# Optimization experiments

Measured on AMD Instinct MI355X. Metric: run time of the kernel, lower is better.

The kernel has to match this reference:

```python
import jax, jax.numpy as jnp
import numpy as np

N, E, IN, H, L, C, K, OPS, B, OUT = 50000, 800000, 64, 128, 3, 4, 32, 7, 512, 10
D = 2 * H * (L + 1)  # classifier in_dim


def _seg_sum(v, idx, n):
    return jax.ops.segment_sum(v, idx, num_segments=n)


def setup_inputs() -> dict:
    key = jax.random.key(0)
    ks = jax.random.split(key, 12)
    s = 0.05
    inp = {}
    inp["x"] = jax.random.normal(ks[0], (N, IN), jnp.float32)
    inp["edge_index"] = jax.random.randint(ks[1], (2, E), 0, N)
    inp["batch"] = jnp.sort(jax.random.randint(ks[2], (N,), 0, B))
    inp["lin1_W"] = jax.random.normal(ks[3], (IN, H), jnp.float32) * s
    inp["lin1_b"] = jnp.zeros((H,), jnp.float32)
    inp["vn0"] = jnp.zeros((H,), jnp.float32)  # virtualnode_embedding init zeros
    inp["W_ops"] = jax.random.normal(ks[4], (L, C, OPS, H, K), jnp.float32) * s
    inp["b_ops"] = jnp.zeros((L, C, OPS, K), jnp.float32)
    inp["att_a"] = jax.random.normal(ks[5], (L, 2, H), jnp.float32) * s
    inp["ln_g"] = jnp.ones((L, C, K), jnp.float32)
    inp["ln_b"] = jnp.zeros((L, C, K), jnp.float32)
    inp["bn_g"] = jnp.ones((L, H), jnp.float32)
    inp["bn_b"] = jnp.zeros((L, H), jnp.float32)
    inp["vn_W1"] = jax.random.normal(ks[6], (L - 1, H, 2 * H), jnp.float32) * s
    inp["vn_b1"] = jnp.zeros((L - 1, 2 * H), jnp.float32)
    inp["vn_bn1_g"] = jnp.ones((L - 1, 2 * H), jnp.float32)
    inp["vn_bn1_b"] = jnp.zeros((L - 1, 2 * H), jnp.float32)
    inp["vn_W2"] = jax.random.normal(ks[7], (L - 1, 2 * H, H), jnp.float32) * s
    inp["vn_b2"] = jnp.zeros((L - 1, H), jnp.float32)
    inp["vn_bn2_g"] = jnp.ones((L - 1, H), jnp.float32)
    inp["vn_bn2_b"] = jnp.zeros((L - 1, H), jnp.float32)
    inp["alphas"] = jax.random.normal(ks[8], (L, C, OPS), jnp.float32)
    inp["head_W"] = jax.random.normal(ks[9], (D, OUT), jnp.float32) * s
    inp["head_b"] = jnp.zeros((OUT,), jnp.float32)
    inp["head_mask"] = jax.random.bernoulli(ks[10], 1.0 / C, (D, OUT)).astype(jnp.float32)
    return inp


def _forward(x, edge_index, batch, lin1_W, lin1_b, vn0, W_ops, b_ops, att_a,
             ln_g, ln_b, bn_g, bn_b, vn_W1, vn_b1, vn_bn1_g, vn_bn1_b,
             vn_W2, vn_b2, vn_bn2_g, vn_bn2_b, alphas, head_W, head_b, head_mask):
    eps = 1e-5
    src, dst = edge_index[0], edge_index[1]
    # atom/feature encoder (mol=False path): elu(lin1(x))
    x = jax.nn.elu(x @ lin1_W + lin1_b)
    # degree / gcn normalization (edge_weights = ones)
    deg = _seg_sum(jnp.ones((E,), x.dtype), dst, N)
    degc = jnp.maximum(deg, 1.0)
    dinv = jax.lax.rsqrt(degc)
    norm = dinv[src] * dinv[dst]
    vn = jnp.tile(vn0[None, :], (B, 1))  # per-graph virtual-node embedding
    gr = [x]
    for l in range(L):
        # virtual-node broadcast-add
        x = x + vn[batch]
        xs = x[src]  # [E,H] gather
        sum_nb = _seg_sum(xs, dst, N)
        mean_nb = sum_nb / degc[:, None]
        norm_agg = _seg_sum(norm[:, None] * xs, dst, N)
        # gat-style segment softmax attention
        e = jax.nn.leaky_relu((x @ att_a[l, 0])[src] + (x @ att_a[l, 1])[dst], 0.2)
        m = jax.ops.segment_max(e, dst, num_segments=N)
        m = jnp.where(jnp.isfinite(m), m, 0.0)
        p = jnp.exp(e - m[dst])
        ssum = _seg_sum(p, dst, N)
        attn_agg = _seg_sum((p / (ssum[dst] + 1e-16))[:, None] * xs, dst, N)
        # 7 primitive aggregations: gcn, gin, gat, sage, graph, arma, mlp
        aggs = jnp.stack([norm_agg, x + sum_nb, attn_agg, x + mean_nb,
                          mean_nb, norm_agg, x])  # [OPS,N,H]
        opmap = jnp.einsum('onh,cohk->ncok', aggs, W_ops[l]) + b_ops[l][None]  # [N,C,OPS,K]
        mu = opmap.mean(-1, keepdims=True)
        var = opmap.var(-1, keepdims=True)
        opmap = (opmap - mu) * jax.lax.rsqrt(var + eps)
        opmap = opmap * ln_g[l][None, :, None, :] + ln_b[l][None, :, None, :]
        w = jax.nn.softmax(alphas[l], -1)  # [C,OPS] DARTS mixing weights
        x = jnp.einsum('ncok,co->nck', opmap, w).reshape(N, H)
        # BatchNorm1d (batch statistics)
        x = (x - x.mean(0)) * jax.lax.rsqrt(x.var(0) + eps) * bn_g[l] + bn_b[l]
        gr.append(x)
        if l < L - 1:
            # virtual-node aggregation + MLP (Linear-BN-ReLU x2)
            vt = _seg_sum(x, batch, B) + vn
            h1 = vt @ vn_W1[l] + vn_b1[l]
            h1 = (h1 - h1.mean(0)) * jax.lax.rsqrt(h1.var(0) + eps) * vn_bn1_g[l] + vn_bn1_b[l]
            h1 = jax.nn.relu(h1)
            h2 = h1 @ vn_W2[l] + vn_b2[l]
            h2 = (h2 - h2.mean(0)) * jax.lax.rsqrt(h2.var(0) + eps) * vn_bn2_g[l] + vn_bn2_b[l]
            vn = jax.nn.relu(h2)
    cat = jnp.concatenate(gr, axis=1)  # [N, H*(L+1)]
    cnt = jnp.maximum(_seg_sum(jnp.ones((N,), cat.dtype), batch, B), 1.0)
    gmean = _seg_sum(cat, batch, B) / cnt[:, None]
    gmax = jax.ops.segment_max(cat, batch, num_segments=B)
    gmax = jnp.where(jnp.isfinite(gmax), gmax, 0.0)
    pooled = jnp.concatenate([gmean, gmax], axis=1)  # [B, D]
    # MixHead: masked linear classifier
    return pooled @ (head_W * head_mask) + head_b


def reference(x, edge_index, batch, lin1_W, lin1_b, vn0, W_ops, b_ops, att_a,
              ln_g, ln_b, bn_g, bn_b, vn_W1, vn_b1, vn_bn1_g, vn_bn1_b,
              vn_W2, vn_b2, vn_bn2_g, vn_bn2_b, alphas, head_W, head_b, head_mask):
    return _forward(x, edge_index, batch, lin1_W, lin1_b, vn0, W_ops, b_ops, att_a,
                    ln_g, ln_b, bn_g, bn_b, vn_W1, vn_b1, vn_bn1_g, vn_bn1_b,
                    vn_W2, vn_b2, vn_bn2_g, vn_bn2_b, alphas, head_W, head_b, head_mask)
```

## Files before the change

kernel.cpp:

```cpp
#include <hip/hip_runtime.h>
#include <math.h>

#define NN 50000
#define EE 800000
#define INF_ 64
#define HH 128
#define LL 3
#define CC 4
#define KK 32
#define OPS_ 7
#define BB 512
#define OUTD 10
#define DD 1024

typedef __attribute__((ext_vector_type(8))) short bf16x8_t;
typedef __attribute__((ext_vector_type(4))) float f32x4_t;

static __device__ inline unsigned short f2bf(float f) {
    unsigned int u = __float_as_uint(f);
    unsigned int r = (u + 0x7fffu + ((u >> 16) & 1u)) >> 16;
    return (unsigned short)r;
}
static __device__ inline unsigned int pack2(float x, float y) {
    return (unsigned int)f2bf(x) | ((unsigned int)f2bf(y) << 16);
}

__global__ __launch_bounds__(256) void k_lin1(const float* __restrict__ x,
                                              const float* __restrict__ W,
                                              const float* __restrict__ b,
                                              float* __restrict__ xout) {
    __shared__ float sW[INF_ * HH];
    __shared__ float sb[HH];
    for (int i = threadIdx.x; i < INF_ * HH; i += 256) sW[i] = W[i];
    if (threadIdx.x < HH) sb[threadIdx.x] = b[threadIdx.x];
    __syncthreads();
    int wave = threadIdx.x >> 6, lane = threadIdx.x & 63;
    int base = blockIdx.x * 64;
    for (int i = 0; i < 16; ++i) {
        int n = base + wave * 16 + i;
        if (n >= NN) break;
        float xv = x[n * INF_ + lane];
        float acc0 = sb[lane], acc1 = sb[lane + 64];
        #pragma unroll 8
        for (int h = 0; h < INF_; ++h) {
            float s = __shfl(xv, h, 64);
            acc0 += s * sW[h * HH + lane];
            acc1 += s * sW[h * HH + lane + 64];
        }
        xout[n * HH + lane]      = acc0 > 0.f ? acc0 : expm1f(acc0);
        xout[n * HH + lane + 64] = acc1 > 0.f ? acc1 : expm1f(acc1);
    }
}

__global__ void k_deg(const int* __restrict__ dst, int* __restrict__ deg) {
    int e = blockIdx.x * 256 + threadIdx.x;
    if (e < EE) atomicAdd(&deg[dst[e]], 1);
}

__global__ void k_alloc(const int* __restrict__ deg, int* __restrict__ off,
                        int* __restrict__ gcount, float* __restrict__ degc,
                        float* __restrict__ dinv) {
    int n = blockIdx.x * 256 + threadIdx.x;
    if (n < NN) {
        int d = deg[n];
        off[n] = atomicAdd(gcount, d);
        float dc = fmaxf((float)d, 1.0f);
        degc[n] = dc;
        dinv[n] = rsqrtf(dc);
    }
}

__global__ void k_csrfill(const int* __restrict__ src, const int* __restrict__ dst,
                          const int* __restrict__ off, int* __restrict__ cursor,
                          int* __restrict__ csr_src) {
    int e = blockIdx.x * 256 + threadIdx.x;
    if (e < EE) {
        int d = dst[e];
        int p = atomicAdd(&cursor[d], 1);
        csr_src[off[d] + p] = src[e];
    }
}

__global__ void k_goff(const int* __restrict__ batch, int* __restrict__ goff) {
    int i = blockIdx.x * 256 + threadIdx.x;
    if (i >= NN) return;
    int b = batch[i];
    if (i == 0) { for (int g = 0; g <= b; ++g) goff[g] = 0; }
    else {
        int bp = batch[i - 1];
        for (int g = bp + 1; g <= b; ++g) goff[g] = i;
    }
    if (i == NN - 1) { for (int g = b + 1; g <= BB; ++g) goff[g] = NN; }
}

__global__ void k_vninit(const float* __restrict__ vn0, float* __restrict__ vn) {
    int i = blockIdx.x * 256 + threadIdx.x;
    if (i < BB * HH) vn[i] = vn0[i & (HH - 1)];
}

__global__ __launch_bounds__(256) void k_addvn_dots(float* __restrict__ x,
                                                    const float* __restrict__ vn,
                                                    const int* __restrict__ batch,
                                                    const float* __restrict__ att,
                                                    float* __restrict__ a0x,
                                                    float* __restrict__ a1x) {
    int wave = threadIdx.x >> 6, lane = threadIdx.x & 63;
    int n = blockIdx.x * 4 + wave;
    if (n >= NN) return;
    int b = batch[n];
    float v0 = x[n * HH + lane]      + vn[b * HH + lane];
    float v1 = x[n * HH + lane + 64] + vn[b * HH + lane + 64];
    x[n * HH + lane] = v0;
    x[n * HH + lane + 64] = v1;
    float d0 = v0 * att[lane] + v1 * att[lane + 64];
    float d1 = v0 * att[HH + lane] + v1 * att[HH + lane + 64];
    #pragma unroll
    for (int s = 32; s; s >>= 1) { d0 += __shfl_xor(d0, s, 64); d1 += __shfl_xor(d1, s, 64); }
    if (lane == 0) { a0x[n] = d0; a1x[n] = d1; }
}

__global__ __launch_bounds__(256) void k_agg(const float* __restrict__ x,
                                             const int* __restrict__ off,
                                             const int* __restrict__ deg,
                                             const int* __restrict__ csr_src,
                                             const float* __restrict__ dinv,
                                             const float* __restrict__ degc,
                                             const float* __restrict__ a0x,
                                             const float* __restrict__ a1x,
                                             unsigned int* __restrict__ An,
                                             unsigned int* __restrict__ Axs,
                                             unsigned int* __restrict__ Aat,
                                             unsigned int* __restrict__ Axm,
                                             unsigned int* __restrict__ Am,
                                             unsigned int* __restrict__ Ax) {
    int wave = threadIdx.x >> 6, lane = threadIdx.x & 63;
    int n = blockIdx.x * 4 + wave;
    if (n >= NN) return;
    int s = off[n], e = s + deg[n];
    float a1n = a1x[n];
    float dinvn = dinv[n];
    float m = -INFINITY;
    for (int j = s + lane; j < e; j += 64) {
        int ss = csr_src[j];
        float ev = a0x[ss] + a1n;
        ev = ev > 0.f ? ev : 0.2f * ev;
        m = fmaxf(m, ev);
    }
    #pragma unroll
    for (int sh = 32; sh; sh >>= 1) m = fmaxf(m, __shfl_xor(m, sh, 64));
    float ls = 0.f;
    for (int j = s + lane; j < e; j += 64) {
        int ss = csr_src[j];
        float ev = a0x[ss] + a1n;
        ev = ev > 0.f ? ev : 0.2f * ev;
        ls += expf(ev - m);
    }
    #pragma unroll
    for (int sh = 32; sh; sh >>= 1) ls += __shfl_xor(ls, sh, 64);
    float sinv = 1.f / (ls + 1e-16f);
    float2 as = {0.f, 0.f}, an = {0.f, 0.f}, aa = {0.f, 0.f};
    const float2* x2 = (const float2*)x;
    for (int j0 = s; j0 < e; j0 += 64) {
        int cnt = min(64, e - j0);
        int ss = (lane < cnt) ? csr_src[j0 + lane] : 0;
        float wn = dinv[ss] * dinvn;
        float ev = a0x[ss] + a1n;
        ev = ev > 0.f ? ev : 0.2f * ev;
        float wa = expf(ev - m) * sinv;
        for (int k = 0; k < cnt; ++k) {
            int sid  = __shfl(ss, k, 64);
            float wnk = __shfl(wn, k, 64);
            float wak = __shfl(wa, k, 64);
            float2 xv = x2[sid * 64 + lane];
            as.x += xv.x;        as.y += xv.y;
            an.x += wnk * xv.x;  an.y += wnk * xv.y;
            aa.x += wak * xv.x;  aa.y += wak * xv.y;
        }
    }
    float2 xv = x2[(size_t)n * 64 + lane];
    float inv_d = 1.f / degc[n];
    int idx = n * 64 + lane;
    An[idx]  = pack2(an.x, an.y);
    Axs[idx] = pack2(xv.x + as.x, xv.y + as.y);
    Aat[idx] = pack2(aa.x, aa.y);
    Axm[idx] = pack2(xv.x + as.x * inv_d, xv.y + as.y * inv_d);
    Am[idx]  = pack2(as.x * inv_d, as.y * inv_d);
    Ax[idx]  = pack2(xv.x, xv.y);
}

__global__ void k_wprep(const float* __restrict__ Wops, unsigned short* __restrict__ wfrag) {
    int idx = blockIdx.x * 256 + threadIdx.x;
    if (idx >= LL * 114688) return;
    int l = idx / 114688, rem = idx % 114688;
    int o = rem / 16384; int r2 = rem % 16384;
    int ct = r2 >> 11; int ks = (r2 >> 9) & 3; int lane = (r2 >> 3) & 63; int j = r2 & 7;
    int h = ks * 32 + (lane >> 4) * 8 + j;
    int col = ct * 16 + (lane & 15);
    int c = col >> 5, kc = col & 31;
    float v = Wops[(((size_t)(l * CC + c) * OPS_ + o) * HH + h) * KK + kc];
    wfrag[idx] = f2bf(v);
}

__global__ void k_sprep(const float* __restrict__ bops, const float* __restrict__ alphas,
                        float* __restrict__ biasf, float* __restrict__ mixw) {
    int idx = blockIdx.x * 256 + threadIdx.x;
    if (idx < LL * OPS_ * HH) {
        int l = idx / 896; int rem = idx % 896;
        int o = rem / 128; int col = rem % 128;
        int c = col >> 5, kc = col & 31;
        biasf[idx] = bops[((l * CC + c) * OPS_ + o) * KK + kc];
    }
    if (idx < LL * CC) {
        int l = idx / CC, c = idx % CC;
        const float* a = alphas + (l * CC + c) * OPS_;
        float mx = -INFINITY;
        for (int o = 0; o < OPS_; ++o) mx = fmaxf(mx, a[o]);
        float s = 0.f, e[OPS_];
        for (int o = 0; o < OPS_; ++o) { e[o] = expf(a[o] - mx); s += e[o]; }
        for (int o = 0; o < OPS_; ++o) mixw[(l * CC + c) * OPS_ + o] = e[o] / s;
    }
}

__global__ __launch_bounds__(256, 3) void k_mixmm(
        const unsigned short* __restrict__ An, const unsigned short* __restrict__ Axs,
        const unsigned short* __restrict__ Aat, const unsigned short* __restrict__ Axm,
        const unsigned short* __restrict__ Am, const unsigned short* __restrict__ Ax,
        const unsigned short* __restrict__ wfrag, const float* __restrict__ biasf,
        const float* __restrict__ lng, const float* __restrict__ lnb,
        const float* __restrict__ mixw,
        float* __restrict__ xnew, float* __restrict__ bnstat) {
    __shared__ unsigned short sB[16384];
    int t = threadIdx.x, w = t >> 6, lane = t & 63;
    int m16 = lane & 15, quad = lane >> 4;
    int nw = blockIdx.x * 128 + w * 32;
    const unsigned short* Aops[OPS_] = {An, Axs, Aat, Axm, Am, An, Ax};
    size_t arow0 = (size_t)min(nw + m16, NN - 1) * HH;
    size_t arow1 = (size_t)min(nw + 16 + m16, NN - 1) * HH;
    float lngv[8], lnbv[8];
    #pragma unroll
    for (int ct = 0; ct < 8; ++ct) { lngv[ct] = lng[ct * 16 + m16]; lnbv[ct] = lnb[ct * 16 + m16]; }
    f32x4_t xacc[2][8];
    #pragma unroll
    for (int i = 0; i < 2; ++i)
        #pragma unroll
        for (int ct = 0; ct < 8; ++ct) xacc[i][ct] = (f32x4_t){0.f, 0.f, 0.f, 0.f};

    for (int o = 0; o < OPS_; ++o) {
        __syncthreads();
        {
            const uint4* gp = (const uint4*)(wfrag + o * 16384);
            uint4* s4 = (uint4*)sB;
            #pragma unroll
            for (int i = 0; i < 8; ++i) s4[t + 256 * i] = gp[t + 256 * i];
        }
        __syncthreads();
        const unsigned short* A = Aops[o];
        bf16x8_t a0[4], a1[4];
        #pragma unroll
        for (int ks = 0; ks < 4; ++ks) {
            a0[ks] = *(const bf16x8_t*)(A + arow0 + ks * 32 + quad * 8);
            a1[ks] = *(const bf16x8_t*)(A + arow1 + ks * 32 + quad * 8);
        }
        #pragma unroll
        for (int g = 0; g < 4; ++g) {
            f32x4_t acc00 = {0.f,0.f,0.f,0.f}, acc01 = {0.f,0.f,0.f,0.f};
            f32x4_t acc10 = {0.f,0.f,0.f,0.f}, acc11 = {0.f,0.f,0.f,0.f};
            #pragma unroll
            for (int ks = 0; ks < 4; ++ks) {
                bf16x8_t b0 = *(const bf16x8_t*)(sB + (2 * g) * 2048 + ks * 512 + lane * 8);
                bf16x8_t b1 = *(const bf16x8_t*)(sB + (2 * g + 1) * 2048 + ks * 512 + lane * 8);
                acc00 = __builtin_amdgcn_mfma_f32_16x16x32_bf16(a0[ks], b0, acc00, 0, 0, 0);
                acc01 = __builtin_amdgcn_mfma_f32_16x16x32_bf16(a0[ks], b1, acc01, 0, 0, 0);
                acc10 = __builtin_amdgcn_mfma_f32_16x16x32_bf16(a1[ks], b0, acc10, 0, 0, 0);
                acc11 = __builtin_amdgcn_mfma_f32_16x16x32_bf16(a1[ks], b1, acc11, 0, 0, 0);
            }
            float wm = mixw[g * OPS_ + o];
            float bv0 = biasf[o * HH + 2 * g * 16 + m16];
            float bv1 = biasf[o * HH + (2 * g + 1) * 16 + m16];
            float wg0 = wm * lngv[2 * g], wg1 = wm * lngv[2 * g + 1];
            float wb0 = wm * lnbv[2 * g], wb1 = wm * lnbv[2 * g + 1];
            #pragma unroll
            for (int r = 0; r < 4; ++r) {
                float v0 = acc00[r] + bv0, v1 = acc01[r] + bv1;
                float s = v0 + v1, q = v0 * v0 + v1 * v1;
                s += __shfl_xor(s, 1); q += __shfl_xor(q, 1);
                s += __shfl_xor(s, 2); q += __shfl_xor(q, 2);
                s += __shfl_xor(s, 4); q += __shfl_xor(q, 4);
                s += __shfl_xor(s, 8); q += __shfl_xor(q, 8);
                float mu = s * (1.f / 32.f);
                float var = fmaxf(q * (1.f / 32.f) - mu * mu, 0.f);
                float rs = rsqrtf(var + 1e-5f);
                xacc[0][2 * g][r]     += (v0 - mu) * rs * wg0 + wb0;
                xacc[0][2 * g + 1][r] += (v1 - mu) * rs * wg1 + wb1;
            }
            #pragma unroll
            for (int r = 0; r < 4; ++r) {
                float v0 = acc10[r] + bv0, v1 = acc11[r] + bv1;
                float s = v0 + v1, q = v0 * v0 + v1 * v1;
                s += __shfl_xor(s, 1); q += __shfl_xor(q, 1);
                s += __shfl_xor(s, 2); q += __shfl_xor(q, 2);
                s += __shfl_xor(s, 4); q += __shfl_xor(q, 4);
                s += __shfl_xor(s, 8); q += __shfl_xor(q, 8);
                float mu = s * (1.f / 32.f);
                float var = fmaxf(q * (1.f / 32.f) - mu * mu, 0.f);
                float rs = rsqrtf(var + 1e-5f);
                xacc[1][2 * g][r]     += (v0 - mu) * rs * wg0 + wb0;
                xacc[1][2 * g + 1][r] += (v1 - mu) * rs * wg1 + wb1;
            }
        }
    }
    #pragma unroll
    for (int ct = 0; ct < 8; ++ct) {
        int col = ct * 16 + m16;
        float ps = 0.f, pq = 0.f;
        #pragma unroll
        for (int tile = 0; tile < 2; ++tile)
            #pragma unroll
            for (int r = 0; r < 4; ++r) {
                int n = nw + tile * 16 + quad * 4 + r;
                if (n < NN) {
                    float v = xacc[tile][ct][r];
                    xnew[(size_t)n * HH + col] = v;
                    ps += v; pq += v * v;
                }
            }
        ps += __shfl_xor(ps, 16); pq += __shfl_xor(pq, 16);
        ps += __shfl_xor(ps, 32); pq += __shfl_xor(pq, 32);
        if (quad == 0) {
            atomicAdd(&bnstat[col], ps);
            atomicAdd(&bnstat[HH + col], pq);
        }
    }
}

__global__ void k_bnfin(const float* __restrict__ stat, const float* __restrict__ g,
                        const float* __restrict__ b, float* __restrict__ scsh,
                        float invn, int dim) {
    int t = threadIdx.x;
    if (t < dim) {
        float mean = stat[t] * invn;
        float var = fmaxf(stat[dim + t] * invn - mean * mean, 0.f);
        float sc = g[t] * rsqrtf(var + 1e-5f);
        scsh[t] = sc;
        scsh[dim + t] = b[t] - mean * sc;
    }
}

__global__ __launch_bounds__(256) void k_pool(const float* __restrict__ src,
                                              const float* __restrict__ scsh,
                                              const int* __restrict__ goff,
                                              float* __restrict__ xout,
                                              float* __restrict__ pooled,
                                              float* __restrict__ gsum, int slice) {
    __shared__ float s1[HH], m1[HH];
    int b = blockIdx.x;
    int f = threadIdx.x & (HH - 1);
    int g = threadIdx.x >> 7;
    int s = goff[b], e = goff[b + 1];
    int cnt = e - s;
    int half = (cnt + 1) >> 1;
    int rs = s + g * half;
    int re = min(e, rs + half);
    float sc = 1.f, sh = 0.f;
    if (scsh) { sc = scsh[f]; sh = scsh[HH + f]; }
    float fs = 0.f, fm = -INFINITY;
    for (int i = rs; i < re; ++i) {
        float v = src[i * HH + f] * sc + sh;
        if (xout) xout[i * HH + f] = v;
        fs += v;
        fm = fmaxf(fm, v);
    }
    if (g == 0) { s1[f] = fs; m1[f] = fm; }
    __syncthreads();
    if (g == 1) {
        fs += s1[f];
        fm = fmaxf(fm, m1[f]);
        float c = fmaxf((float)cnt, 1.f);
        pooled[b * DD + slice * HH + f] = fs / c;
        pooled[b * DD + 512 + slice * HH + f] = (cnt > 0) ? fm : 0.f;
        if (gsum) gsum[b * HH + f] = fs;
    }
}

__global__ void k_vn1(const float* __restrict__ gsum, const float* __restrict__ vn,
                      const float* __restrict__ W1, const float* __restrict__ b1,
                      float* __restrict__ h1, float* __restrict__ stat) {
    __shared__ float row[HH];
    int b = blockIdx.x, t = threadIdx.x;
    if (t < HH) row[t] = gsum[b * HH + t] + vn[b * HH + t];
    __syncthreads();
    float acc = b1[t];
    for (int h = 0; h < HH; ++h) acc += row[h] * W1[h * 2 * HH + t];
    h1[b * 2 * HH + t] = acc;
    atomicAdd(&stat[t], acc);
    atomicAdd(&stat[2 * HH + t], acc * acc);
}

__global__ void k_vn2(const float* __restrict__ h1, const float* __restrict__ scsh1,
                      const float* __restrict__ W2, const float* __restrict__ b2,
                      float* __restrict__ h2, float* __restrict__ stat) {
    __shared__ float row[2 * HH];
    int b = blockIdx.x, t = threadIdx.x;
    float v = h1[b * 2 * HH + t] * scsh1[t] + scsh1[2 * HH + t];
    row[t] = fmaxf(v, 0.f);
    __syncthreads();
    if (t < HH) {
        float acc = b2[t];
        for (int h = 0; h < 2 * HH; ++h) acc += row[h] * W2[h * HH + t];
        h2[b * HH + t] = acc;
        atomicAdd(&stat[t], acc);
        atomicAdd(&stat[HH + t], acc * acc);
    }
}

__global__ void k_vnout(const float* __restrict__ h2, const float* __restrict__ scsh2,
                        float* __restrict__ vn) {
    int i = blockIdx.x * 256 + threadIdx.x;
    if (i < BB * HH) {
        int f = i & (HH - 1);
        float v = h2[i] * scsh2[f] + scsh2[HH + f];
        vn[i] = fmaxf(v, 0.f);
    }
}

__global__ void k_head(const float* __restrict__ pooled, const float* __restrict__ W,
                       const float* __restrict__ bias, const float* __restrict__ mask,
                       float* __restrict__ out) {
    int wave = threadIdx.x >> 6, lane = threadIdx.x & 63;
    int idx = blockIdx.x * 4 + wave;
    if (idx >= BB * OUTD) return;
    int b = idx / OUTD, o = idx % OUTD;
    float acc = 0.f;
    for (int k = lane; k < DD; k += 64)
        acc += pooled[b * DD + k] * W[k * OUTD + o] * mask[k * OUTD + o];
    #pragma unroll
    for (int sh = 32; sh; sh >>= 1) acc += __shfl_xor(acc, sh, 64);
    if (lane == 0) out[idx] = acc + bias[o];
}

extern "C" void kernel_launch(void* const* d_in, const int* in_sizes, int n_in,
                              void* d_out, int out_size, void* d_ws, size_t ws_size,
                              hipStream_t stream) {
    const float* x_in   = (const float*)d_in[0];
    const int*   ei     = (const int*)d_in[1];
    const int*   batch  = (const int*)d_in[2];
    const float* lin1W  = (const float*)d_in[3];
    const float* lin1b  = (const float*)d_in[4];
    const float* vn0    = (const float*)d_in[5];
    const float* Wops   = (const float*)d_in[6];
    const float* bops   = (const float*)d_in[7];
    const float* atta   = (const float*)d_in[8];
    const float* lng    = (const float*)d_in[9];
    const float* lnb    = (const float*)d_in[10];
    const float* bng    = (const float*)d_in[11];
    const float* bnb    = (const float*)d_in[12];
    const float* vnW1   = (const float*)d_in[13];
    const float* vnb1   = (const float*)d_in[14];
    const float* vnbn1g = (const float*)d_in[15];
    const float* vnbn1b = (const float*)d_in[16];
    const float* vnW2   = (const float*)d_in[17];
    const float* vnb2   = (const float*)d_in[18];
    const float* vnbn2g = (const float*)d_in[19];
    const float* vnbn2b = (const float*)d_in[20];
    const float* alphas = (const float*)d_in[21];
    const float* headW  = (const float*)d_in[22];
    const float* headb  = (const float*)d_in[23];
    const float* headm  = (const float*)d_in[24];
    float* out = (float*)d_out;
    const int* src = ei;
    const int* dst = ei + EE;

    float* ws = (float*)d_ws;
    size_t p = 0;
    float* xcur    = ws + p; p += (size_t)NN * HH;
    float* a0x     = ws + p; p += NN;
    float* a1x     = ws + p; p += NN;
    float* degc    = ws + p; p += NN;
    float* dinv    = ws + p; p += NN;
    float* vn      = ws + p; p += BB * HH;
    float* gsum    = ws + p; p += BB * HH;
    float* h1      = ws + p; p += BB * 2 * HH;
    float* h2      = ws + p; p += BB * HH;
    float* pooled  = ws + p; p += (size_t)BB * DD;
    float* bnscsh  = ws + p; p += LL * 2 * HH;
    float* vnsc1   = ws + p; p += 2 * 2 * (2 * HH);
    float* vnsc2   = ws + p; p += 2 * 2 * HH;
    float* biasf   = ws + p; p += LL * OPS_ * HH;
    float* mixw    = ws + p; p += LL * CC * OPS_;
    unsigned int* An  = (unsigned int*)(ws + p); p += (size_t)NN * 64;
    unsigned int* Axs = (unsigned int*)(ws + p); p += (size_t)NN * 64;
    unsigned int* Aat = (unsigned int*)(ws + p); p += (size_t)NN * 64;
    unsigned int* Axm = (unsigned int*)(ws + p); p += (size_t)NN * 64;
    unsigned int* Am  = (unsigned int*)(ws + p); p += (size_t)NN * 64;
    unsigned int* Ax  = (unsigned int*)(ws + p); p += (size_t)NN * 64;
    unsigned short* wfrag = (unsigned short*)(ws + p); p += (LL * 114688) / 2;
    float* zf = ws + p;
    float* bnstat  = ws + p; p += LL * 2 * HH;
    float* vnstat1 = ws + p; p += 2 * 2 * (2 * HH);
    float* vnstat2 = ws + p; p += 2 * 2 * HH;
    size_t zf_cnt = (size_t)((ws + p) - zf);
    int* ib = (int*)(ws + p);
    int* deg    = ib;
    int* gcount = ib + NN;
    int* cursor = ib + NN + 1;
    size_t zi_cnt = (size_t)(2 * NN + 1);
    int* off    = ib + 2 * NN + 1;
    int* goff   = off + NN;
    int* csr    = goff + (BB + 1);

    hipMemsetAsync(zf, 0, zf_cnt * sizeof(float), stream);
    hipMemsetAsync(ib, 0, zi_cnt * sizeof(int), stream);

    k_lin1<<<(NN + 63) / 64, 256, 0, stream>>>(x_in, lin1W, lin1b, xcur);
    k_deg<<<(EE + 255) / 256, 256, 0, stream>>>(dst, deg);
    k_alloc<<<(NN + 255) / 256, 256, 0, stream>>>(deg, off, gcount, degc, dinv);
    k_csrfill<<<(EE + 255) / 256, 256, 0, stream>>>(src, dst, off, cursor, csr);
    k_goff<<<(NN + 255) / 256, 256, 0, stream>>>(batch, goff);
    k_vninit<<<(BB * HH + 255) / 256, 256, 0, stream>>>(vn0, vn);
    k_wprep<<<(LL * 114688 + 255) / 256, 256, 0, stream>>>(Wops, wfrag);
    k_sprep<<<(LL * OPS_ * HH + 255) / 256, 256, 0, stream>>>(bops, alphas, biasf, mixw);
    k_pool<<<BB, 256, 0, stream>>>(xcur, nullptr, goff, nullptr, pooled, nullptr, 0);

    for (int l = 0; l < LL; ++l) {
        k_addvn_dots<<<NN / 4, 256, 0, stream>>>(xcur, vn, batch, atta + l * 2 * HH, a0x, a1x);
        k_agg<<<NN / 4, 256, 0, stream>>>(xcur, off, deg, csr, dinv, degc, a0x, a1x,
                                          An, Axs, Aat, Axm, Am, Ax);
        k_mixmm<<<(NN + 127) / 128, 256, 0, stream>>>(
            (const unsigned short*)An, (const unsigned short*)Axs,
            (const unsigned short*)Aat, (const unsigned short*)Axm,
            (const unsigned short*)Am, (const unsigned short*)Ax,
            wfrag + (size_t)l * 114688, biasf + l * OPS_ * HH,
            lng + l * HH, lnb + l * HH, mixw + l * CC * OPS_,
            xcur, bnstat + l * 2 * HH);
        k_bnfin<<<1, 128, 0, stream>>>(bnstat + l * 2 * HH, bng + l * HH, bnb + l * HH,
                                       bnscsh + l * 2 * HH, 1.0f / (float)NN, HH);
        k_pool<<<BB, 256, 0, stream>>>(xcur, bnscsh + l * 2 * HH, goff, xcur, pooled,
                                       (l < LL - 1) ? gsum : nullptr, l + 1);
        if (l < LL - 1) {
            k_vn1<<<BB, 256, 0, stream>>>(gsum, vn, vnW1 + (size_t)l * HH * 2 * HH,
                                          vnb1 + l * 2 * HH, h1, vnstat1 + l * 2 * (2 * HH));
            k_bnfin<<<1, 256, 0, stream>>>(vnstat1 + l * 2 * (2 * HH), vnbn1g + l * 2 * HH,
                                           vnbn1b + l * 2 * HH, vnsc1 + l * 2 * (2 * HH),
                                           1.0f / (float)BB, 2 * HH);
            k_vn2<<<BB, 256, 0, stream>>>(h1, vnsc1 + l * 2 * (2 * HH),
                                          vnW2 + (size_t)l * 2 * HH * HH, vnb2 + l * HH,
                                          h2, vnstat2 + l * 2 * HH);
            k_bnfin<<<1, 128, 0, stream>>>(vnstat2 + l * 2 * HH, vnbn2g + l * HH,
                                           vnbn2b + l * HH, vnsc2 + l * 2 * HH,
                                           1.0f / (float)BB, HH);
            k_vnout<<<(BB * HH + 255) / 256, 256, 0, stream>>>(h2, vnsc2 + l * 2 * HH, vn);
        }
    }
    k_head<<<(BB * OUTD) / 4, 256, 0, stream>>>(pooled, headW, headb, headm, out);
}
```

Baseline: 1.265 ms.

## Add fast path in aggregation for nodes with at most 64 neighbours

For nodes with degree up to 64, the aggregation kernel now computes the attention softmax in a single pass over one register-held batch of neighbours, instead of three passes that each re-read the CSR indices. The gather is split so the two half-waves each load a different neighbour row as float4. The halves are combined with a cross-half shuffle, and the six packed output stores are divided between the two halves using 8-byte writes. Higher-degree nodes keep the old path, which adds branch divergence and code size.

```diff
diff --git a/kernel.cpp b/kernel.cpp
--- a/kernel.cpp
+++ b/kernel.cpp
@@ -23,6 +23,9 @@
 }
 static __device__ inline unsigned int pack2(float x, float y) {
     return (unsigned int)f2bf(x) | ((unsigned int)f2bf(y) << 16);
+}
+static __device__ inline uint2 pack4(float a, float b, float c, float d) {
+    uint2 r; r.x = pack2(a, b); r.y = pack2(c, d); return r;
 }
 
 __global__ __launch_bounds__(256) void k_lin1(const float* __restrict__ x,
@@ -136,56 +139,108 @@
     int wave = threadIdx.x >> 6, lane = threadIdx.x & 63;
     int n = blockIdx.x * 4 + wave;
     if (n >= NN) return;
-    int s = off[n], e = s + deg[n];
-    float a1n = a1x[n];
-    float dinvn = dinv[n];
-    float m = -INFINITY;
-    for (int j = s + lane; j < e; j += 64) {
-        int ss = csr_src[j];
+    int s = off[n], d = deg[n];
+    float a1n = a1x[n], dinvn = dinv[n];
+    int hh = lane >> 5, fl = lane & 31;
+    float4 as4 = {0.f,0.f,0.f,0.f}, an4 = {0.f,0.f,0.f,0.f}, aa4 = {0.f,0.f,0.f,0.f};
+    const float4* x4 = (const float4*)x;
+
+    if (d > 0 && d <= 64) {
+        int ss = csr_src[s + min(lane, d - 1)];
+        bool act = lane < d;
         float ev = a0x[ss] + a1n;
         ev = ev > 0.f ? ev : 0.2f * ev;
-        m = fmaxf(m, ev);
-    }
-    #pragma unroll
-    for (int sh = 32; sh; sh >>= 1) m = fmaxf(m, __shfl_xor(m, sh, 64));
-    float ls = 0.f;
-    for (int j = s + lane; j < e; j += 64) {
-        int ss = csr_src[j];
-        float ev = a0x[ss] + a1n;
-        ev = ev > 0.f ? ev : 0.2f * ev;
-        ls += expf(ev - m);
-    }
-    #pragma unroll
-    for (int sh = 32; sh; sh >>= 1) ls += __shfl_xor(ls, sh, 64);
-    float sinv = 1.f / (ls + 1e-16f);
-    float2 as = {0.f, 0.f}, an = {0.f, 0.f}, aa = {0.f, 0.f};
-    const float2* x2 = (const float2*)x;
-    for (int j0 = s; j0 < e; j0 += 64) {
-        int cnt = min(64, e - j0);
-        int ss = (lane < cnt) ? csr_src[j0 + lane] : 0;
+        float m = act ? ev : -INFINITY;
+        #pragma unroll
+        for (int sh = 32; sh; sh >>= 1) m = fmaxf(m, __shfl_xor(m, sh, 64));
+        float pv = act ? expf(ev - m) : 0.f;
+        float ls = pv;
+        #pragma unroll
+        for (int sh = 32; sh; sh >>= 1) ls += __shfl_xor(ls, sh, 64);
+        float wa = pv / (ls + 1e-16f);
         float wn = dinv[ss] * dinvn;
-        float ev = a0x[ss] + a1n;
-        ev = ev > 0.f ? ev : 0.2f * ev;
-        float wa = expf(ev - m) * sinv;
-        for (int k = 0; k < cnt; ++k) {
-            int sid  = __shfl(ss, k, 64);
-            float wnk = __shfl(wn, k, 64);
-            float wak = __shfl(wa, k, 64);
-            float2 xv = x2[sid * 64 + lane];
-            as.x += xv.x;        as.y += xv.y;
-            an.x += wnk * xv.x;  an.y += wnk * xv.y;
-            aa.x += wak * xv.x;  aa.y += wak * xv.y;
-        }
-    }
-    float2 xv = x2[(size_t)n * 64 + lane];
+        for (int k2 = 0; k2 < d; k2 += 2) {
+            int kk = min(k2 + hh, d - 1);
+            int sid  = __shfl(ss, kk, 64);
+            float wnk = __shfl(wn, kk, 64);
+            float wak = __shfl(wa, kk, 64);
+            float4 xv = x4[(size_t)sid * 32 + fl];
+            if (k2 + hh < d) {
+                as4.x += xv.x; as4.y += xv.y; as4.z += xv.z; as4.w += xv.w;
+                an4.x += wnk * xv.x; an4.y += wnk * xv.y; an4.z += wnk * xv.z; an4.w += wnk * xv.w;
+                aa4.x += wak * xv.x; aa4.y += wak * xv.y; aa4.z += wak * xv.z; aa4.w += wak * xv.w;
+            }
+        }
+        as4.x += __shfl_xor(as4.x, 32, 64); as4.y += __shfl_xor(as4.y, 32, 64);
+        as4.z += __shfl_xor(as4.z, 32, 64); as4.w += __shfl_xor(as4.w, 32, 64);
+        an4.x += __shfl_xor(an4.x, 32, 64); an4.y += __shfl_xor(an4.y, 32, 64);
+        an4.z += __shfl_xor(an4.z, 32, 64); an4.w += __shfl_xor(an4.w, 32, 64);
+        aa4.x += __shfl_xor(aa4.x, 32, 64); aa4.y += __shfl_xor(aa4.y, 32, 64);
+        aa4.z += __shfl_xor(aa4.z, 32, 64); aa4.w += __shfl_xor(aa4.w, 32, 64);
+    } else if (d > 0) {
+        int e = s + d;
+        float m = -INFINITY;
+        for (int j = s + lane; j < e; j += 64) {
+            int ss = csr_src[j];
+            float ev = a0x[ss] + a1n;
+            ev = ev > 0.f ? ev : 0.2f * ev;
+            m = fmaxf(m, ev);
+        }
+        #pragma unroll
+        for (int sh = 32; sh; sh >>= 1) m = fmaxf(m, __shfl_xor(m, sh, 64));
+        float ls = 0.f;
+        for (int j = s + lane; j < e; j += 64) {
+            int ss = csr_src[j];
+            float ev = a0x[ss] + a1n;
+            ev = ev > 0.f ? ev : 0.2f * ev;
+            ls += expf(ev - m);
+        }
+        #pragma unroll
+        for (int sh = 32; sh; sh >>= 1) ls += __shfl_xor(ls, sh, 64);
+        float sinv = 1.f / (ls + 1e-16f);
+        float2 as = {0.f, 0.f}, an = {0.f, 0.f}, aa = {0.f, 0.f};
+        const float2* x2 = (const float2*)x;
+        for (int j0 = s; j0 < e; j0 += 64) {
+            int cnt = min(64, e - j0);
+            int ss = (lane < cnt) ? csr_src[j0 + lane] : 0;
+            float wn = dinv[ss] * dinvn;
+            float ev = a0x[ss] + a1n;
+            ev = ev > 0.f ? ev : 0.2f * ev;
+            float wap = expf(ev - m) * sinv;
+            for (int k = 0; k < cnt; ++k) {
+                int sid  = __shfl(ss, k, 64);
+                float wnk = __shfl(wn, k, 64);
+                float wak = __shfl(wap, k, 64);
+                float2 xv = x2[sid * 64 + lane];
+                as.x += xv.x;        as.y += xv.y;
+                an.x += wnk * xv.x;  an.y += wnk * xv.y;
+                aa.x += wak * xv.x;  aa.y += wak * xv.y;
+            }
+        }
+        float2 xv = x2[(size_t)n * 64 + lane];
+        float inv_d = 1.f / degc[n];
+        int idx = n * 64 + lane;
+        An[idx]  = pack2(an.x, an.y);
+        Axs[idx] = pack2(xv.x + as.x, xv.y + as.y);
+        Aat[idx] = pack2(aa.x, aa.y);
+        Axm[idx] = pack2(xv.x + as.x * inv_d, xv.y + as.y * inv_d);
+        Am[idx]  = pack2(as.x * inv_d, as.y * inv_d);
+        Ax[idx]  = pack2(xv.x, xv.y);
+        return;
+    }
+    float4 xself = x4[(size_t)n * 32 + fl];
     float inv_d = 1.f / degc[n];
-    int idx = n * 64 + lane;
-    An[idx]  = pack2(an.x, an.y);
-    Axs[idx] = pack2(xv.x + as.x, xv.y + as.y);
-    Aat[idx] = pack2(aa.x, aa.y);
-    Axm[idx] = pack2(xv.x + as.x * inv_d, xv.y + as.y * inv_d);
-    Am[idx]  = pack2(as.x * inv_d, as.y * inv_d);
-    Ax[idx]  = pack2(xv.x, xv.y);
+    size_t oi = (size_t)n * 32 + fl;
+    if (hh == 0) {
+        ((uint2*)An)[oi]  = pack4(an4.x, an4.y, an4.z, an4.w);
+        ((uint2*)Axs)[oi] = pack4(xself.x + as4.x, xself.y + as4.y, xself.z + as4.z, xself.w + as4.w);
+        ((uint2*)Aat)[oi] = pack4(aa4.x, aa4.y, aa4.z, aa4.w);
+    } else {
+        ((uint2*)Axm)[oi] = pack4(xself.x + as4.x * inv_d, xself.y + as4.y * inv_d,
+                                  xself.z + as4.z * inv_d, xself.w + as4.w * inv_d);
+        ((uint2*)Am)[oi]  = pack4(as4.x * inv_d, as4.y * inv_d, as4.z * inv_d, as4.w * inv_d);
+        ((uint2*)Ax)[oi]  = pack4(xself.x, xself.y, xself.z, xself.w);
+    }
 }
 
 __global__ void k_wprep(const float* __restrict__ Wops, unsigned short* __restrict__ wfrag) {
```

Result: faster. 1.228 ms (-3.0%).
